# Kernel optimization log

Hardware: AMD Instinct MI355X
Metric: run time of the kernel (lower is better)

## Reference

```python
import jax, jax.numpy as jnp
import numpy as np

B, QLEN, MLEN, C, H = 2, 1024, 1024, 1024, 16
DK = C // H
KLEN = QLEN + MLEN


def setup_inputs() -> dict:
    key0 = jax.random.key(0)
    ks = jax.random.split(key0, 11)
    w_scale = 1.0 / np.sqrt(C)
    return {
        "key": jax.random.normal(ks[0], (B, KLEN, C), jnp.float32),
        "query": jax.random.normal(ks[1], (B, QLEN, C), jnp.float32),
        "pos_embs": jax.random.normal(ks[2], (KLEN, 1, C), jnp.float32),
        "mask": jnp.ones((B, 1, QLEN, KLEN), jnp.int32),
        "u_bias": jax.random.normal(ks[3], (H, DK), jnp.float32) * 0.02,
        "v_bias": jax.random.normal(ks[4], (H, DK), jnp.float32) * 0.02,
        "Wk": jax.random.normal(ks[5], (C, C), jnp.float32) * w_scale,
        "Wv": jax.random.normal(ks[6], (C, C), jnp.float32) * w_scale,
        "Wq": jax.random.normal(ks[7], (C, C), jnp.float32) * w_scale,
        "Wo": jax.random.normal(ks[8], (C, C), jnp.float32) * w_scale,
        "Wp": jax.random.normal(ks[9], (C, C), jnp.float32) * w_scale,
    }


def _rel_shift(x):
    # x: [B, qlen, klen, H] -> Transformer-XL pad/reshape shift trick
    b, q, k, h = x.shape
    xp = jnp.pad(x, ((0, 0), (0, 0), (1, 0), (0, 0)))       # [B, q, k+1, H]
    xp = xp.reshape(b, k + 1, q, h)[:, 1:]                   # [B, k, q, H]
    return xp.reshape(b, q, k, h)


def reference(key, query, pos_embs, mask, u_bias, v_bias, Wk, Wv, Wq, Wo, Wp):
    bs, qlen = query.shape[:2]
    klen = key.shape[1]
    n_heads, d_k = u_bias.shape
    scale = jnp.sqrt(jnp.asarray(d_k, key.dtype))

    k = (key @ Wk.T).reshape(bs, klen, n_heads, d_k)
    v = (key @ Wv.T).reshape(bs, klen, n_heads, d_k)
    # NOTE: original module projects key[:, -qlen:] (not `query`) as queries.
    q = (key[:, -qlen:] @ Wq.T).reshape(bs, qlen, n_heads, d_k)
    p = (pos_embs @ Wp.T).reshape(-1, n_heads, d_k)          # [klen, H, d_k]

    AC = jnp.einsum('bihd,bjhd->bijh', q + u_bias[None, None], k)
    BD = jnp.einsum('bihd,jhd->bijh', q + v_bias[None, None], p)
    BD = _rel_shift(BD)
    e = (AC + BD) / scale                                    # [B, q, k, H]

    m = mask[:, 0, :, :, None]                               # squeeze(1).unsqueeze(-1)
    e = jnp.where(m == 0, jnp.finfo(e.dtype).min, e)

    aw = jax.nn.softmax(e, axis=2)                           # softmax over klen
    cv = jnp.einsum('bijh,bjhd->bihd', aw, v).reshape(bs, qlen, n_heads * d_k)
    cv = cv @ Wo.T
    return cv, aw.transpose(0, 3, 1, 2)
```

## Files before the change

### kernel.cpp

```cpp
#include <hip/hip_runtime.h>
#include <hip/hip_bf16.h>


typedef __hip_bfloat16 bf16;
typedef __attribute__((ext_vector_type(8))) short bf16x8v;
typedef __attribute__((ext_vector_type(4))) float f32x4;

#define MFMA16(A, B, C) __builtin_amdgcn_mfma_f32_16x16x32_bf16(A, B, C, 0, 0, 0)

#define QL 1024
#define KL 2048
#define NH 16
#define DKD 64
#define CD 1024

static __device__ __forceinline__ unsigned short f2bf(float x) {
  __hip_bfloat16 h = __float2bfloat16(x);
  return __builtin_bit_cast(unsigned short, h);
}
static __device__ __forceinline__ float bf2f(unsigned short u) {
  return __builtin_bit_cast(float, (unsigned)u << 16);
}

typedef const __attribute__((address_space(1))) void* gptr_t;
typedef __attribute__((address_space(3))) void* sptr_t;


__global__ void cast_all(const float* __restrict__ key, const float* __restrict__ pos,
                         const float* __restrict__ wk, const float* __restrict__ wv,
                         const float* __restrict__ wq, const float* __restrict__ wp,
                         const float* __restrict__ wo,
                         bf16* __restrict__ keyb, bf16* __restrict__ qsrc,
                         bf16* __restrict__ posb, bf16* __restrict__ wkvb,
                         bf16* __restrict__ wqpb, bf16* __restrict__ wob) {
  const int bid = blockIdx.x;
  if (bid < 4096) {
    int i = (bid * 256 + threadIdx.x) * 4;
    float4 v = *(const float4*)(key + i);
    ushort4 o;
    o.x = f2bf(v.x); o.y = f2bf(v.y); o.z = f2bf(v.z); o.w = f2bf(v.w);
    *(ushort4*)((unsigned short*)keyb + i) = o;
    int row = i >> 10;
    int col = i & (CD - 1);
    int r2 = row & (KL - 1);
    if (r2 >= QL) {
      int qrow = (row >> 11) * QL + (r2 - QL);
      *(ushort4*)((unsigned short*)qsrc + (size_t)qrow * CD + col) = o;
    }
    return;
  }
  const int mb = bid - 4096;
  const float* src;
  bf16* dst;
  int cb;
  if (mb < 2048)      { src = pos; dst = posb;           cb = mb; }
  else if (mb < 3072) { src = wk;  dst = wkvb;           cb = mb - 2048; }
  else if (mb < 4096) { src = wv;  dst = wkvb + (1<<20); cb = mb - 3072; }
  else if (mb < 5120) { src = wq;  dst = wqpb;           cb = mb - 4096; }
  else if (mb < 6144) { src = wp;  dst = wqpb + (1<<20); cb = mb - 5120; }
  else                { src = wo;  dst = wob;            cb = mb - 6144; }
  int i = cb * 1024 + threadIdx.x * 4;
  float4 v = *(const float4*)(src + i);
  ushort4 o;
  o.x = f2bf(v.x); o.y = f2bf(v.y); o.z = f2bf(v.z); o.w = f2bf(v.w);
  *(ushort4*)((unsigned short*)dst + i) = o;
}


template <int MODE>
__global__ __launch_bounds__(256) void gemm_bt(
    const bf16* __restrict__ Ain, const bf16* __restrict__ A2,
    const bf16* __restrict__ Btin,
    void* __restrict__ O1, void* __restrict__ O2, void* __restrict__ O3,
    const float* __restrict__ bias1, const float* __restrict__ bias2,
    int M, int N, int K) {
  __shared__ __align__(16) bf16 As[128 * 32];
  __shared__ __align__(16) bf16 Bs[128 * 32];
  const int tid = threadIdx.x;
  const int lane = tid & 63;
  const int wid = tid >> 6;
  const int wr = wid >> 1, wc = wid & 1;
  const int lrow = lane & 15, lk = lane >> 4;
  const int m0 = blockIdx.x * 128, n0 = blockIdx.y * 128;

  const bf16* A = Ain;
  const bf16* Bt = Btin;
  if (MODE == 5) {
    if (blockIdx.z) { A = A2; Bt = Btin + (size_t)(1 << 20); }
  }

  f32x4 acc[4][4];
#pragma unroll
  for (int i = 0; i < 4; i++)
#pragma unroll
    for (int j = 0; j < 4; j++) acc[i][j] = (f32x4){0.f, 0.f, 0.f, 0.f};

  for (int k0 = 0; k0 < K; k0 += 32) {
#pragma unroll
    for (int st = 0; st < 2; ++st) {
      int c = st * 256 + tid;
      __builtin_amdgcn_global_load_lds(
          (gptr_t)(A + (size_t)(m0 + (c >> 2)) * K + k0 + (c & 3) * 8),
          (sptr_t)(As + c * 8), 16, 0, 0);
      __builtin_amdgcn_global_load_lds(
          (gptr_t)(Bt + (size_t)(n0 + (c >> 2)) * K + k0 + (c & 3) * 8),
          (sptr_t)(Bs + c * 8), 16, 0, 0);
    }
    __syncthreads();
    bf16x8v aF[4], bF[4];
#pragma unroll
    for (int s = 0; s < 4; s++) {
      aF[s] = *(const bf16x8v*)(As + (wr * 64 + s * 16 + lrow) * 32 + lk * 8);
      bF[s] = *(const bf16x8v*)(Bs + (wc * 64 + s * 16 + lrow) * 32 + lk * 8);
    }
#pragma unroll
    for (int i = 0; i < 4; i++)
#pragma unroll
      for (int j = 0; j < 4; j++) acc[i][j] = MFMA16(aF[i], bF[j], acc[i][j]);
    __syncthreads();
  }

  const int row0 = m0 + wr * 64 + lk * 4;
  const int col0 = n0 + wc * 64 + lrow;

  if (MODE == 1) {
    float* C = (float*)O1;
#pragma unroll
    for (int i = 0; i < 4; i++)
#pragma unroll
      for (int j = 0; j < 4; j++) {
        int r = row0 + i * 16, c = col0 + j * 16;
#pragma unroll
        for (int q = 0; q < 4; q++) C[(size_t)(r + q) * N + c] = acc[i][j][q];
      }
  } else if (MODE == 4) {
    if (n0 < 1024) {
      bf16* C = (bf16*)O1;
#pragma unroll
      for (int i = 0; i < 4; i++)
#pragma unroll
        for (int j = 0; j < 4; j++) {
          int c = col0 + j * 16;
          const int hh = c >> 6, dd = c & 63;
#pragma unroll
          for (int q = 0; q < 4; q++) {
            int m = row0 + i * 16 + q;
            const int bb = m >> 11, jj = m & (KL - 1);
            C[((size_t)(bb * NH + hh) * KL + jj) * DKD + dd] = __float2bfloat16(acc[i][j][q]);
          }
        }
    } else {
      unsigned short* C = (unsigned short*)O2;
#pragma unroll
      for (int i = 0; i < 4; i++)
#pragma unroll
        for (int j = 0; j < 4; j++) {
          int m = row0 + i * 16;
          int c = col0 + j * 16 - 1024;
          int bb = m >> 11;
          int jj = m & (KL - 1);
          int bhh = bb * NH + (c >> 6);
          int dd = c & (DKD - 1);
          ushort4 o;
          o.x = f2bf(acc[i][j][0]); o.y = f2bf(acc[i][j][1]);
          o.z = f2bf(acc[i][j][2]); o.w = f2bf(acc[i][j][3]);
          *(ushort4*)(C + (size_t)(bhh * DKD + dd) * KL + jj) = o;
        }
    }
  } else {
    if (blockIdx.z == 0) {
      bf16* C1 = (bf16*)O1;
      bf16* C2 = (bf16*)O2;
#pragma unroll
      for (int i = 0; i < 4; i++)
#pragma unroll
        for (int j = 0; j < 4; j++) {
          int r = row0 + i * 16, c = col0 + j * 16;
          float b1 = bias1[c], b2 = bias2[c];
#pragma unroll
          for (int q = 0; q < 4; q++) {
            float v = acc[i][j][q];
            C1[(size_t)(r + q) * CD + c] = __float2bfloat16(v + b1);
            C2[(size_t)(r + q) * CD + c] = __float2bfloat16(v + b2);
          }
        }
    } else {
      bf16* C = (bf16*)O3;
#pragma unroll
      for (int i = 0; i < 4; i++)
#pragma unroll
        for (int j = 0; j < 4; j++) {
          int r = row0 + i * 16, c = col0 + j * 16;
#pragma unroll
          for (int q = 0; q < 4; q++) C[(size_t)(r + q) * CD + c] = __float2bfloat16(acc[i][j][q]);
        }
    }
  }
}


__global__ __launch_bounds__(256) void bd_gemm(
    const bf16* __restrict__ qvb, const bf16* __restrict__ Pbuf,
    unsigned short* __restrict__ BDsh) {
  __shared__ __align__(16) bf16 As[128 * 32];
  __shared__ __align__(16) bf16 Bs[128 * 32];
  const int tid = threadIdx.x;
  const int lane = tid & 63;
  const int wid = tid >> 6;
  const int wr = wid >> 1, wc = wid & 1;
  const int lrow = lane & 15, lk = lane >> 4;
  const int m0 = blockIdx.x * 128, n0 = blockIdx.y * 128;
  const int bh = blockIdx.z, b = bh >> 4, h = bh & 15;

  const bf16* A = qvb + (size_t)(b * QL + m0) * CD + h * DKD;
  const bf16* Bt = Pbuf + (size_t)n0 * CD + h * DKD;

  f32x4 acc[4][4];
#pragma unroll
  for (int i = 0; i < 4; i++)
#pragma unroll
    for (int j = 0; j < 4; j++) acc[i][j] = (f32x4){0.f, 0.f, 0.f, 0.f};

#pragma unroll
  for (int k0 = 0; k0 < 64; k0 += 32) {
#pragma unroll
    for (int st = 0; st < 2; ++st) {
      int c = st * 256 + tid;
      __builtin_amdgcn_global_load_lds(
          (gptr_t)(A + (size_t)(c >> 2) * CD + k0 + (c & 3) * 8),
          (sptr_t)(As + c * 8), 16, 0, 0);
      __builtin_amdgcn_global_load_lds(
          (gptr_t)(Bt + (size_t)(c >> 2) * CD + k0 + (c & 3) * 8),
          (sptr_t)(Bs + c * 8), 16, 0, 0);
    }
    __syncthreads();
    bf16x8v aF[4], bF[4];
#pragma unroll
    for (int s = 0; s < 4; s++) {
      aF[s] = *(const bf16x8v*)(As + (wr * 64 + s * 16 + lrow) * 32 + lk * 8);
      bF[s] = *(const bf16x8v*)(Bs + (wc * 64 + s * 16 + lrow) * 32 + lk * 8);
    }
#pragma unroll
    for (int i = 0; i < 4; i++)
#pragma unroll
      for (int j = 0; j < 4; j++) acc[i][j] = MFMA16(aF[i], bF[j], acc[i][j]);
    __syncthreads();
  }

  unsigned short* out = BDsh + (size_t)bh * QL * KL;
  const int row0 = m0 + wr * 64 + lk * 4;
  const int col0 = n0 + wc * 64 + lrow;
#pragma unroll
  for (int i = 0; i < 4; i++)
#pragma unroll
    for (int j = 0; j < 4; j++) {
      const int cg = col0 + j * 16;
#pragma unroll
      for (int q = 0; q < 4; q++) {
        const int il = row0 + i * 16 + q;
        const int thr = 1023 - il;
        unsigned short val = f2bf(acc[i][j][q]);
        if (cg >= thr) {
          out[(size_t)il * KL + (cg - thr)] = val;
        } else if (il >= 1) {
          out[(size_t)(il - 1) * KL + il + 1025 + cg] = val;
        }
      }
    }
}


__global__ __launch_bounds__(512) void attn_fused(
    const bf16* __restrict__ qu, const unsigned short* __restrict__ Kp,
    const unsigned short* __restrict__ BDsh, const unsigned short* __restrict__ Vt,
    float* __restrict__ aw, bf16* __restrict__ cvb) {
  __shared__ __align__(16) char smraw[49664];
  float* ssum = (float*)(smraw + 49152);
  unsigned short* pt = (unsigned short*)(smraw + 32768);
  float* cvl = (float*)smraw;

  const int bid = blockIdx.x;
  const int xcd = bid & 7;
  const int kk = bid >> 3;
  const int bh = xcd * 4 + (kk >> 5);
  const int pair = kk & 31;
  const int i0p = pair * 32;
  const int b = bh >> 4, h = bh & 15;
  const int tid = threadIdx.x;
  const int lane = tid & 63, wid = tid >> 6;
  const int tile = wid >> 2, wq = wid & 3;
  const int lrow = lane & 15, lk = lane >> 4;
  const int i0 = i0p + tile * 16;
  const int irow = i0 + lrow;

  const size_t qoff = (size_t)(b * QL + irow) * CD + h * DKD + lk * 8;
  const bf16x8v quF0 = *(const bf16x8v*)(qu + qoff);
  const bf16x8v quF1 = *(const bf16x8v*)(qu + qoff + 32);

  const unsigned short* Kph = Kp + (size_t)bh * KL * DKD;
  const unsigned short* BDrow = BDsh + (size_t)(bh * QL + i0p) * KL;
  const unsigned short* Vth = Vt + (size_t)bh * DKD * KL;
  float* awp = aw + (size_t)(bh * QL + irow) * KL;

  ushort4 pst[32];
  float lacc = 0.f;

  auto stageA = [&](int cc, int bsel) {
#pragma unroll
    for (int st = 0; st < 2; ++st) {
      const int pos = (st * 512 + tid) * 16;
      const int krow = pos >> 7;
      const int kb = (pos & 127) ^ ((krow & 7) << 4);
      __builtin_amdgcn_global_load_lds(
          (gptr_t)(Kph + (size_t)(cc * 128 + krow) * DKD + (kb >> 1)),
          (sptr_t)(smraw + bsel * 16384 + pos), 16, 0, 0);
    }
    {
      const int pos = tid * 16;
      const int brow = pos >> 8;
      const int bb2 = (pos & 255) ^ ((brow & 7) << 4);
      __builtin_amdgcn_global_load_lds(
          (gptr_t)(BDrow + (size_t)brow * KL + cc * 128 + (bb2 >> 1)),
          (sptr_t)(smraw + 32768 + bsel * 8192 + pos), 16, 0, 0);
    }
  };

  auto stageV = [&](int cc, int bsel) {
#pragma unroll
    for (int st = 0; st < 2; ++st) {
      const int pos = (st * 512 + tid) * 16;
      const int vrow = pos >> 8;
      const int vb = (pos & 255) ^ ((vrow & 7) << 4);
      __builtin_amdgcn_global_load_lds(
          (gptr_t)(Vth + (size_t)vrow * KL + cc * 128 + (vb >> 1)),
          (sptr_t)(smraw + bsel * 16384 + pos), 16, 0, 0);
    }
  };

  stageA(0, 0);
#pragma unroll
  for (int c = 0; c < 16; ++c) {
    const int cur = c & 1;
    if (c < 15) {
      stageA(c + 1, cur ^ 1);
      asm volatile("s_waitcnt vmcnt(3)" ::: "memory");
    } else {
      asm volatile("s_waitcnt vmcnt(0)" ::: "memory");
    }
    __builtin_amdgcn_sched_barrier(0);
    __builtin_amdgcn_s_barrier();

    const char* Kc = (const char*)smraw + cur * 16384;
    const char* BDc = (const char*)smraw + 32768 + cur * 8192;
#pragma unroll
    for (int s2 = 0; s2 < 2; ++s2) {
      const int jloc = wq * 32 + s2 * 16 + lrow;
      const int sw = (jloc & 7) << 4;
      const bf16x8v kF0 = *(const bf16x8v*)(Kc + jloc * 128 + ((lk * 16) ^ sw));
      const bf16x8v kF1 = *(const bf16x8v*)(Kc + jloc * 128 + ((64 + lk * 16) ^ sw));
      f32x4 ac = (f32x4){0.f, 0.f, 0.f, 0.f};
      __builtin_amdgcn_s_setprio(1);
      ac = MFMA16(kF0, quF0, ac);
      ac = MFMA16(kF1, quF1, ac);
      __builtin_amdgcn_s_setprio(0);

      const int bdb = (tile * 16 + lrow) * 256 +
                      ((wq * 64 + s2 * 32 + lk * 8) ^ ((lrow & 7) << 4));
      const ushort4 bd4 = *(const ushort4*)(BDc + bdb);
      const unsigned short* bdp = (const unsigned short*)&bd4;
      ushort4 pb;
      unsigned short* pp = (unsigned short*)&pb;
#pragma unroll
      for (int q = 0; q < 4; ++q) {
        const int jcol = c * 128 + wq * 32 + s2 * 16 + lk * 4 + q;
        const float bd = (jcol - irow == 1025) ? 0.f : bf2f(bdp[q]);
        const float pu = __expf((ac[q] + bd) * 0.125f);
        lacc += pu;
        pp[q] = f2bf(pu);
      }
      pst[c * 2 + s2] = pb;
    }
    __builtin_amdgcn_s_barrier();
  }

  lacc += __shfl_xor(lacc, 16);
  lacc += __shfl_xor(lacc, 32);
  if (lane < 16) ssum[wid * 16 + lane] = lacc;
  __syncthreads();
  const float sc =
      1.0f / (ssum[(tile * 4 + 0) * 16 + lrow] + ssum[(tile * 4 + 1) * 16 + lrow] +
              ssum[(tile * 4 + 2) * 16 + lrow] + ssum[(tile * 4 + 3) * 16 + lrow]);
  __syncthreads();

  f32x4 cvacc[4];
#pragma unroll
  for (int dd = 0; dd < 4; ++dd) cvacc[dd] = (f32x4){0.f, 0.f, 0.f, 0.f};

  unsigned short* ptw = pt + ((tile * 4 + wq) * 16 + lrow) * 40;

  stageV(0, 0);
#pragma unroll
  for (int c = 0; c < 16; ++c) {
    const int cur = c & 1;
    if (c < 15) stageV(c + 1, cur ^ 1);
    if (c == 0)      asm volatile("s_waitcnt vmcnt(2)" ::: "memory");
    else if (c < 15) asm volatile("s_waitcnt vmcnt(4)" ::: "memory");
    else             asm volatile("s_waitcnt vmcnt(2)" ::: "memory");
    __builtin_amdgcn_sched_barrier(0);
    __builtin_amdgcn_s_barrier();

#pragma unroll
    for (int s2 = 0; s2 < 2; ++s2) {
      const unsigned short* pp = (const unsigned short*)&pst[c * 2 + s2];
      const float p0 = bf2f(pp[0]) * sc;
      const float p1 = bf2f(pp[1]) * sc;
      const float p2 = bf2f(pp[2]) * sc;
      const float p3 = bf2f(pp[3]) * sc;
      f32x4 o4 = (f32x4){p0, p1, p2, p3};
      __builtin_nontemporal_store(
          o4, (f32x4*)(awp + c * 128 + wq * 32 + s2 * 16 + lk * 4));
      ushort4 pb2;
      pb2.x = f2bf(p0); pb2.y = f2bf(p1); pb2.z = f2bf(p2); pb2.w = f2bf(p3);
      *(ushort4*)(ptw + s2 * 16 + lk * 4) = pb2;
    }
    const bf16x8v aF = *(const bf16x8v*)(ptw + lk * 8);
    const char* Vc = (const char*)smraw + cur * 16384;
    __builtin_amdgcn_s_setprio(1);
#pragma unroll
    for (int dd = 0; dd < 4; ++dd) {
      const int vr = dd * 16 + lrow;
      const bf16x8v vF =
          *(const bf16x8v*)(Vc + vr * 256 + ((wq * 64 + lk * 16) ^ ((vr & 7) << 4)));
      cvacc[dd] = MFMA16(aF, vF, cvacc[dd]);
    }
    __builtin_amdgcn_s_setprio(0);
    __builtin_amdgcn_s_barrier();
  }

#pragma unroll
  for (int dd = 0; dd < 4; ++dd)
#pragma unroll
    for (int q = 0; q < 4; ++q)
      cvl[tile * 4224 + ((wq * 16 + lk * 4 + q) * 66) + dd * 16 + lrow] = cvacc[dd][q];
  __syncthreads();
#pragma unroll
  for (int t4 = 0; t4 < 4; ++t4) {
    const int idx = tid + t4 * 512;
    const int row32 = idx >> 6, dk = idx & 63;
    const int tr = row32 >> 4, row = row32 & 15;
    const float v = cvl[tr * 4224 + ((0 * 16 + row) * 66) + dk] +
                    cvl[tr * 4224 + ((1 * 16 + row) * 66) + dk] +
                    cvl[tr * 4224 + ((2 * 16 + row) * 66) + dk] +
                    cvl[tr * 4224 + ((3 * 16 + row) * 66) + dk];
    cvb[(size_t)(b * QL + i0p + row32) * CD + h * DKD + dk] = __float2bfloat16(v);
  }
}


extern "C" void kernel_launch(void* const* d_in, const int* in_sizes, int n_in,
                              void* d_out, int out_size, void* d_ws, size_t ws_size,
                              hipStream_t stream) {
  const float* key = (const float*)d_in[0];
  const float* pos = (const float*)d_in[2];
  const float* ub = (const float*)d_in[4];
  const float* vb = (const float*)d_in[5];
  const float* Wk = (const float*)d_in[6];
  const float* Wv = (const float*)d_in[7];
  const float* Wq = (const float*)d_in[8];
  const float* Wo = (const float*)d_in[9];
  const float* Wp = (const float*)d_in[10];

  char* ws = (char*)d_ws;
  size_t off = 0;
  bf16* keyb = (bf16*)(ws + off); off += (size_t)4096 * 1024 * 2;
  bf16* qsrc = (bf16*)(ws + off); off += (size_t)2048 * 1024 * 2;
  bf16* posb = (bf16*)(ws + off); off += (size_t)2048 * 1024 * 2;
  bf16* wkvb = (bf16*)(ws + off); off += (size_t)2048 * 1024 * 2;
  bf16* wqpb = (bf16*)(ws + off); off += (size_t)2048 * 1024 * 2;
  bf16* wob  = (bf16*)(ws + off); off += (size_t)1024 * 1024 * 2;
  bf16* Kp   = (bf16*)(ws + off); off += (size_t)4096 * 1024 * 2;
  bf16* Vt   = (bf16*)(ws + off); off += (size_t)4096 * 1024 * 2;
  bf16* qu   = (bf16*)(ws + off); off += (size_t)2048 * 1024 * 2;
  bf16* qvb  = (bf16*)(ws + off); off += (size_t)2048 * 1024 * 2;
  bf16* Pbuf = (bf16*)(ws + off); off += (size_t)2048 * 1024 * 2;
  bf16* cvb  = (bf16*)(ws + off); off += (size_t)2048 * 1024 * 2;
  unsigned short* BDsh = (unsigned short*)(ws + off); off += (size_t)32 * QL * KL * 2;

  float* cv_out = (float*)d_out;
  float* aw_out = (float*)d_out + (size_t)2 * QL * CD;

  cast_all<<<11264, 256, 0, stream>>>(key, pos, Wk, Wv, Wq, Wp, Wo,
                                      keyb, qsrc, posb, wkvb, wqpb, wob);

  gemm_bt<4><<<dim3(32, 16), 256, 0, stream>>>(keyb, nullptr, wkvb, Kp, Vt, nullptr,
                                               nullptr, nullptr, 4096, 2048, 1024);
  gemm_bt<5><<<dim3(16, 8, 2), 256, 0, stream>>>(qsrc, posb, wqpb, qu, qvb, Pbuf,
                                                 ub, vb, 2048, 1024, 1024);

  bd_gemm<<<dim3(8, 16, 32), 256, 0, stream>>>(qvb, Pbuf, BDsh);

  attn_fused<<<1024, 512, 0, stream>>>(qu, (const unsigned short*)Kp, BDsh,
                                       (const unsigned short*)Vt, aw_out, cvb);

  gemm_bt<1><<<dim3(16, 8), 256, 0, stream>>>(cvb, nullptr, wob, cv_out, nullptr, nullptr,
                                              nullptr, nullptr, 2048, 1024, 1024);
}
```

Measured before the change: 259.1 us.

## Fuse PV accumulation into score loop with deferred softmax normalization

Merges the two passes of the attention kernel into one. V tiles now load alongside K and BD each chunk, and unnormalized bf16 probabilities feed straight into 16x16x16 MFMAs from registers, with no LDS round trip for the P tile. The softmax normalization is applied once at the end to the context output, and the attention-weight stores are issued after the loop. This removes the second pass over V, its pipeline and barriers, but uses 80KB of LDS (lower occupancy), half-width MFMAs, and multiplies unnormalized P by V.

```diff
diff --git a/kernel.cpp b/kernel.cpp
--- a/kernel.cpp
+++ b/kernel.cpp
@@ -4,9 +4,11 @@
 
 typedef __hip_bfloat16 bf16;
 typedef __attribute__((ext_vector_type(8))) short bf16x8v;
+typedef __attribute__((ext_vector_type(4))) short bf16x4v;
 typedef __attribute__((ext_vector_type(4))) float f32x4;
 
 #define MFMA16(A, B, C) __builtin_amdgcn_mfma_f32_16x16x32_bf16(A, B, C, 0, 0, 0)
+#define MFMA16H(A, B, C) __builtin_amdgcn_mfma_f32_16x16x16bf16_1k(A, B, C, 0, 0, 0)
 
 #define QL 1024
 #define KL 2048
@@ -274,10 +276,9 @@
     const bf16* __restrict__ qu, const unsigned short* __restrict__ Kp,
     const unsigned short* __restrict__ BDsh, const unsigned short* __restrict__ Vt,
     float* __restrict__ aw, bf16* __restrict__ cvb) {
-  __shared__ __align__(16) char smraw[49664];
-  float* ssum = (float*)(smraw + 49152);
-  unsigned short* pt = (unsigned short*)(smraw + 32768);
+  __shared__ __align__(16) char smraw[81920];
   float* cvl = (float*)smraw;
+  float* ssum = (float*)(smraw + 33792);
 
   const int bid = blockIdx.x;
   const int xcd = bid & 7;
@@ -302,7 +303,7 @@
   const unsigned short* Vth = Vt + (size_t)bh * DKD * KL;
   float* awp = aw + (size_t)(bh * QL + irow) * KL;
 
-  ushort4 pst[32];
+  bf16x4v pst[32];
   float lacc = 0.f;
 
   auto stageA = [&](int cc, int bsel) {
@@ -323,9 +324,6 @@
           (gptr_t)(BDrow + (size_t)brow * KL + cc * 128 + (bb2 >> 1)),
           (sptr_t)(smraw + 32768 + bsel * 8192 + pos), 16, 0, 0);
     }
-  };
-
-  auto stageV = [&](int cc, int bsel) {
 #pragma unroll
     for (int st = 0; st < 2; ++st) {
       const int pos = (st * 512 + tid) * 16;
@@ -333,9 +331,13 @@
       const int vb = (pos & 255) ^ ((vrow & 7) << 4);
       __builtin_amdgcn_global_load_lds(
           (gptr_t)(Vth + (size_t)vrow * KL + cc * 128 + (vb >> 1)),
-          (sptr_t)(smraw + bsel * 16384 + pos), 16, 0, 0);
+          (sptr_t)(smraw + 49152 + bsel * 16384 + pos), 16, 0, 0);
     }
   };
+
+  f32x4 cvacc[4];
+#pragma unroll
+  for (int dd = 0; dd < 4; ++dd) cvacc[dd] = (f32x4){0.f, 0.f, 0.f, 0.f};
 
   stageA(0, 0);
 #pragma unroll
@@ -343,7 +345,7 @@
     const int cur = c & 1;
     if (c < 15) {
       stageA(c + 1, cur ^ 1);
-      asm volatile("s_waitcnt vmcnt(3)" ::: "memory");
+      asm volatile("s_waitcnt vmcnt(5)" ::: "memory");
     } else {
       asm volatile("s_waitcnt vmcnt(0)" ::: "memory");
     }
@@ -352,6 +354,8 @@
 
     const char* Kc = (const char*)smraw + cur * 16384;
     const char* BDc = (const char*)smraw + 32768 + cur * 8192;
+    const char* Vc = (const char*)smraw + 49152 + cur * 16384;
+
 #pragma unroll
     for (int s2 = 0; s2 < 2; ++s2) {
       const int jloc = wq * 32 + s2 * 16 + lrow;
@@ -368,7 +372,7 @@
                       ((wq * 64 + s2 * 32 + lk * 8) ^ ((lrow & 7) << 4));
       const ushort4 bd4 = *(const ushort4*)(BDc + bdb);
       const unsigned short* bdp = (const unsigned short*)&bd4;
-      ushort4 pb;
+      bf16x4v pb;
       unsigned short* pp = (unsigned short*)&pb;
 #pragma unroll
       for (int q = 0; q < 4; ++q) {
@@ -380,6 +384,19 @@
       }
       pst[c * 2 + s2] = pb;
     }
+
+    __builtin_amdgcn_s_setprio(1);
+#pragma unroll
+    for (int dd = 0; dd < 4; ++dd) {
+      const int vr = dd * 16 + lrow;
+#pragma unroll
+      for (int s2 = 0; s2 < 2; ++s2) {
+        const bf16x4v vF = *(const bf16x4v*)(
+            Vc + vr * 256 + ((wq * 64 + s2 * 32 + lk * 8) ^ ((vr & 7) << 4)));
+        cvacc[dd] = MFMA16H(pst[c * 2 + s2], vF, cvacc[dd]);
+      }
+    }
+    __builtin_amdgcn_s_setprio(0);
     __builtin_amdgcn_s_barrier();
   }
 
@@ -390,52 +407,6 @@
   const float sc =
       1.0f / (ssum[(tile * 4 + 0) * 16 + lrow] + ssum[(tile * 4 + 1) * 16 + lrow] +
               ssum[(tile * 4 + 2) * 16 + lrow] + ssum[(tile * 4 + 3) * 16 + lrow]);
-  __syncthreads();
-
-  f32x4 cvacc[4];
-#pragma unroll
-  for (int dd = 0; dd < 4; ++dd) cvacc[dd] = (f32x4){0.f, 0.f, 0.f, 0.f};
-
-  unsigned short* ptw = pt + ((tile * 4 + wq) * 16 + lrow) * 40;
-
-  stageV(0, 0);
-#pragma unroll
-  for (int c = 0; c < 16; ++c) {
-    const int cur = c & 1;
-    if (c < 15) stageV(c + 1, cur ^ 1);
-    if (c == 0)      asm volatile("s_waitcnt vmcnt(2)" ::: "memory");
-    else if (c < 15) asm volatile("s_waitcnt vmcnt(4)" ::: "memory");
-    else             asm volatile("s_waitcnt vmcnt(2)" ::: "memory");
-    __builtin_amdgcn_sched_barrier(0);
-    __builtin_amdgcn_s_barrier();
-
-#pragma unroll
-    for (int s2 = 0; s2 < 2; ++s2) {
-      const unsigned short* pp = (const unsigned short*)&pst[c * 2 + s2];
-      const float p0 = bf2f(pp[0]) * sc;
-      const float p1 = bf2f(pp[1]) * sc;
-      const float p2 = bf2f(pp[2]) * sc;
-      const float p3 = bf2f(pp[3]) * sc;
-      f32x4 o4 = (f32x4){p0, p1, p2, p3};
-      __builtin_nontemporal_store(
-          o4, (f32x4*)(awp + c * 128 + wq * 32 + s2 * 16 + lk * 4));
-      ushort4 pb2;
-      pb2.x = f2bf(p0); pb2.y = f2bf(p1); pb2.z = f2bf(p2); pb2.w = f2bf(p3);
-      *(ushort4*)(ptw + s2 * 16 + lk * 4) = pb2;
-    }
-    const bf16x8v aF = *(const bf16x8v*)(ptw + lk * 8);
-    const char* Vc = (const char*)smraw + cur * 16384;
-    __builtin_amdgcn_s_setprio(1);
-#pragma unroll
-    for (int dd = 0; dd < 4; ++dd) {
-      const int vr = dd * 16 + lrow;
-      const bf16x8v vF =
-          *(const bf16x8v*)(Vc + vr * 256 + ((wq * 64 + lk * 16) ^ ((vr & 7) << 4)));
-      cvacc[dd] = MFMA16(aF, vF, cvacc[dd]);
-    }
-    __builtin_amdgcn_s_setprio(0);
-    __builtin_amdgcn_s_barrier();
-  }
 
 #pragma unroll
   for (int dd = 0; dd < 4; ++dd)
@@ -448,11 +419,28 @@
     const int idx = tid + t4 * 512;
     const int row32 = idx >> 6, dk = idx & 63;
     const int tr = row32 >> 4, row = row32 & 15;
+    const float sinv =
+        1.0f / (ssum[(tr * 4 + 0) * 16 + row] + ssum[(tr * 4 + 1) * 16 + row] +
+                ssum[(tr * 4 + 2) * 16 + row] + ssum[(tr * 4 + 3) * 16 + row]);
     const float v = cvl[tr * 4224 + ((0 * 16 + row) * 66) + dk] +
                     cvl[tr * 4224 + ((1 * 16 + row) * 66) + dk] +
                     cvl[tr * 4224 + ((2 * 16 + row) * 66) + dk] +
                     cvl[tr * 4224 + ((3 * 16 + row) * 66) + dk];
-    cvb[(size_t)(b * QL + i0p + row32) * CD + h * DKD + dk] = __float2bfloat16(v);
+    cvb[(size_t)(b * QL + i0p + row32) * CD + h * DKD + dk] =
+        __float2bfloat16(v * sinv);
+  }
+
+#pragma unroll
+  for (int ii = 0; ii < 32; ++ii) {
+    const int cc = ii >> 1, s2 = ii & 1;
+    const unsigned short* pp = (const unsigned short*)&pst[ii];
+    f32x4 o4;
+    o4[0] = bf2f(pp[0]) * sc;
+    o4[1] = bf2f(pp[1]) * sc;
+    o4[2] = bf2f(pp[2]) * sc;
+    o4[3] = bf2f(pp[3]) * sc;
+    __builtin_nontemporal_store(
+        o4, (f32x4*)(awp + cc * 128 + wq * 32 + s2 * 16 + lk * 4));
   }
 }
 
```

New measurement: 263.7 us. About the same (+1.8%).
